# Performance work log

Measured on AMD Instinct MI355X. Metric: run time of the kernel, lower is better.

The kernel has to match this reference:

```python
import jax, jax.numpy as jnp
import numpy as np

D_MODEL = 1024
NUM_HEADS = 16
HEAD_DIM = D_MODEL // NUM_HEADS


def setup_inputs() -> dict:
    key = jax.random.key(0)
    k_x, k_wqkv, k_bqkv, k_wo, k_bo = jax.random.split(key, 5)
    s = 1.0 / np.sqrt(D_MODEL)
    return {
        "x": jax.random.normal(k_x, (4, 2048, D_MODEL), dtype=jnp.float32),
        "W_qkv": jax.random.uniform(k_wqkv, (D_MODEL, 3 * D_MODEL), jnp.float32, -s, s),
        "b_qkv": jax.random.uniform(k_bqkv, (3 * D_MODEL,), jnp.float32, -s, s),
        "W_out": jax.random.uniform(k_wo, (D_MODEL, D_MODEL), jnp.float32, -s, s),
        "b_out": jax.random.uniform(k_bo, (D_MODEL,), jnp.float32, -s, s),
    }


def reference(x, W_qkv, b_qkv, W_out, b_out):
    B, N, C = x.shape
    # fused QKV projection -> [B, N, 3, H, Dh]
    qkv = (x @ W_qkv + b_qkv).reshape(B, N, 3, NUM_HEADS, HEAD_DIM)
    q = jnp.transpose(qkv[:, :, 0], (0, 2, 1, 3))  # [B, H, N, Dh]
    k = jnp.transpose(qkv[:, :, 1], (0, 2, 1, 3))
    v = jnp.transpose(qkv[:, :, 2], (0, 2, 1, 3))
    scale = 1.0 / jnp.sqrt(jnp.asarray(HEAD_DIM, dtype=x.dtype))
    attn = jnp.einsum('bhqd,bhkd->bhqk', q, k) * scale  # [B, H, N, N]
    attn = jax.nn.softmax(attn, axis=-1)
    # dropout is identity in eval mode
    out = jnp.einsum('bhqk,bhkd->bhqd', attn, v)  # [B, H, N, Dh]
    out = jnp.transpose(out, (0, 2, 1, 3)).reshape(B, N, C)
    return out @ W_out + b_out
```

## Files before the change

kernel.cpp:

```cpp
#include <hip/hip_runtime.h>


typedef __bf16 bf16x8 __attribute__((ext_vector_type(8)));
typedef float f32x4 __attribute__((ext_vector_type(4)));
typedef unsigned int u32x4 __attribute__((ext_vector_type(4)));

#define DEV __device__ __forceinline__

DEV unsigned short f2b(float x) {
  unsigned int u = __float_as_uint(x);
  u += 0x7fffu + ((u >> 16) & 1u);
  return (unsigned short)(u >> 16);
}

DEV unsigned int pk2(float a, float b) {
  union { __bf16 h[2]; unsigned int u; } c;
  c.h[0] = (__bf16)a;
  c.h[1] = (__bf16)b;
  return c.u;
}

#if __has_builtin(__builtin_amdgcn_exp2f)
DEV float exp2_fast(float x) { return __builtin_amdgcn_exp2f(x); }
#else
DEV float exp2_fast(float x) { return exp2f(x); }
#endif

DEV void xpose_pair(unsigned int a, unsigned int b,
                    unsigned int& x, unsigned int& y) {
#if __has_builtin(__builtin_amdgcn_permlane32_swap) && \
    __has_builtin(__builtin_amdgcn_permlane16_swap)
  auto t = __builtin_amdgcn_permlane32_swap(a, b, false, false);
  auto u = __builtin_amdgcn_permlane16_swap(t[0], t[1], false, false);
  x = u[0];
  y = u[1];
#else
  int la = (int)(threadIdx.x & 63);
  unsigned int a32 = (unsigned int)__shfl_xor((int)a, 32, 64);
  unsigned int b32 = (unsigned int)__shfl_xor((int)b, 32, 64);
  unsigned int t0 = (la < 32) ? a : b32;
  unsigned int t1 = (la < 32) ? a32 : b;
  unsigned int t0x = (unsigned int)__shfl_xor((int)t0, 16, 64);
  unsigned int t1x = (unsigned int)__shfl_xor((int)t1, 16, 64);
  bool odd = ((la >> 4) & 1) != 0;
  x = odd ? t1x : t0;
  y = odd ? t1 : t0x;
#endif
}

DEV bf16x8 u4_to_bf(u32x4 v) {
  union { u32x4 u; bf16x8 b; } c;
  c.u = v;
  return c.b;
}

DEV void g2l16(const void* g, void* l) {
  __builtin_amdgcn_global_load_lds(
      (const __attribute__((address_space(1))) unsigned int*)(unsigned long long)g,
      (__attribute__((address_space(3))) unsigned int*)(unsigned int)(unsigned long long)l,
      16, 0, 0);
}

__global__ void cvt_x_kernel(const float* __restrict__ x,
                             unsigned short* __restrict__ xb) {
  int i = blockIdx.x * blockDim.x + threadIdx.x;
  float4 v = ((const float4*)x)[i];
  ushort4 o;
  o.x = f2b(v.x); o.y = f2b(v.y); o.z = f2b(v.z); o.w = f2b(v.w);
  ((ushort4*)xb)[i] = o;
}

__global__ void cvt_wt_kernel(const float* __restrict__ W,
                              unsigned short* __restrict__ Wt,
                              int K, int N) {
  __shared__ float tile[32][33];
  int n0 = blockIdx.x * 32, k0 = blockIdx.y * 32;
  int tx = threadIdx.x, ty = threadIdx.y;
#pragma unroll
  for (int i = 0; i < 32; i += 8)
    tile[ty + i][tx] = W[(size_t)(k0 + ty + i) * N + n0 + tx];
  __syncthreads();
#pragma unroll
  for (int i = 0; i < 32; i += 8)
    Wt[(size_t)(n0 + ty + i) * K + k0 + tx] = f2b(tile[tx][ty + i]);
}

#define QSCALE 0.18033688011112042f

template <int MODE>
__global__ __launch_bounds__(256, 2)
void gemm_bt_kernel(const unsigned short* __restrict__ A,
                    const unsigned short* __restrict__ Bt,
                    const float* __restrict__ bias,
                    unsigned short* __restrict__ qout,
                    unsigned short* __restrict__ kfrout,
                    unsigned short* __restrict__ vfrout,
                    float* __restrict__ fout) {
  constexpr int K = 1024;
  __shared__ unsigned short As[128 * 32];
  __shared__ unsigned short Bs[128 * 32];

  const int tid = threadIdx.x;
  const int lane = tid & 63;
  const int w = tid >> 6;
  const int wm = w & 1, wn = w >> 1;
  const int l15 = lane & 15, quad = lane >> 4;
  const int m0 = blockIdx.y * 128;
  const int n0 = blockIdx.x * 128;

  const unsigned short* Ag = A + (size_t)m0 * K;
  const unsigned short* Bg = Bt + (size_t)n0 * K;

  const int c0 = tid, c1 = tid + 256;
  const size_t ga0 = (size_t)(c0 >> 2) * K + (size_t)(c0 & 3) * 8;
  const size_t ga1 = (size_t)(c1 >> 2) * K + (size_t)(c1 & 3) * 8;
  unsigned short* la0 = &As[c0 * 8];
  unsigned short* la1 = &As[c1 * 8];
  unsigned short* lb0 = &Bs[c0 * 8];
  unsigned short* lb1 = &Bs[c1 * 8];

  f32x4 acc[4][4] = {};

  for (int kt = 0; kt < K; kt += 32) {
    g2l16(Ag + ga0 + kt, la0);
    g2l16(Ag + ga1 + kt, la1);
    g2l16(Bg + ga0 + kt, lb0);
    g2l16(Bg + ga1 + kt, lb1);
    __syncthreads();
    bf16x8 af[4], bfr[4];
#pragma unroll
    for (int i = 0; i < 4; ++i) {
      af[i]  = *(const bf16x8*)&As[(wm * 64 + i * 16 + l15) * 32 + quad * 8];
      bfr[i] = *(const bf16x8*)&Bs[(wn * 64 + i * 16 + l15) * 32 + quad * 8];
    }
#pragma unroll
    for (int mi = 0; mi < 4; ++mi)
#pragma unroll
      for (int ni = 0; ni < 4; ++ni)
        acc[mi][ni] = __builtin_amdgcn_mfma_f32_16x16x32_bf16(
            af[mi], bfr[ni], acc[mi][ni], 0, 0, 0);
    __syncthreads();
  }

  float bv[4];
#pragma unroll
  for (int ni = 0; ni < 4; ++ni)
    bv[ni] = bias[n0 + wn * 64 + ni * 16 + l15];

  if (MODE == 0) {
    const int sel = n0 >> 10;
    const int bbat = m0 >> 11;
    const int ktb = ((m0 & 2047) >> 6) + wm;
    if (sel == 0) {
#pragma unroll
      for (int mi = 0; mi < 4; ++mi) {
        int rb = m0 + wm * 64 + mi * 16 + quad * 4;
#pragma unroll
        for (int ni = 0; ni < 4; ++ni) {
          int c = (n0 & 1023) + wn * 64 + ni * 16 + l15;
#pragma unroll
          for (int r = 0; r < 4; ++r)
            qout[(size_t)(rb + r) * 1024 + c] =
                f2b((acc[mi][ni][r] + bv[ni]) * QSCALE);
        }
      }
    } else if (sel == 1) {
#pragma unroll
      for (int ni = 0; ni < 4; ++ni) {
        int c = (n0 & 1023) + wn * 64 + ni * 16 + l15;
        int h = c >> 6, d = c & 63;
        int kc = d >> 5, dq = (d >> 3) & 3, j = d & 7;
        size_t fb = ((((size_t)(bbat * 16 + h) * 32 + ktb) * 8) + kc) * 512 +
                    (size_t)(dq * 16) * 8 + j;
#pragma unroll
        for (int mi = 0; mi < 4; ++mi) {
          size_t fm = fb + (size_t)mi * 1024;
#pragma unroll
          for (int r = 0; r < 4; ++r)
            kfrout[fm + (quad * 4 + r) * 8] = f2b(acc[mi][ni][r] + bv[ni]);
        }
      }
    } else {
      const int fqb = quad >> 1;
      const int jj0 = (quad & 1) * 4;
#pragma unroll
      for (int ni = 0; ni < 4; ++ni) {
        int c = (n0 & 1023) + wn * 64 + ni * 16 + l15;
        int h = c >> 6, d = c & 63;
        int df = d >> 4, fl15 = d & 15;
#pragma unroll
        for (int mi = 0; mi < 4; ++mi) {
          int kc2 = mi >> 1;
          int fquad = (mi & 1) * 2 + fqb;
          size_t fb = ((((size_t)(bbat * 16 + h) * 32 + ktb) * 8) + df * 2 + kc2) * 512 +
                      (size_t)(fquad * 16 + fl15) * 8 + jj0;
          ushort4 pk;
          pk.x = f2b(acc[mi][ni][0] + bv[ni]);
          pk.y = f2b(acc[mi][ni][1] + bv[ni]);
          pk.z = f2b(acc[mi][ni][2] + bv[ni]);
          pk.w = f2b(acc[mi][ni][3] + bv[ni]);
          *(ushort4*)&vfrout[fb] = pk;
        }
      }
    }
  } else {
#pragma unroll
    for (int mi = 0; mi < 4; ++mi) {
      int rb = m0 + wm * 64 + mi * 16 + quad * 4;
#pragma unroll
      for (int ni = 0; ni < 4; ++ni) {
        int c = n0 + wn * 64 + ni * 16 + l15;
#pragma unroll
        for (int r = 0; r < 4; ++r)
          fout[(size_t)(rb + r) * 1024 + c] = acc[mi][ni][r] + bv[ni];
      }
    }
  }
}

__global__ __launch_bounds__(512, 1)
void attn_kernel(const unsigned short* __restrict__ qg,
                 const unsigned short* __restrict__ kfr,
                 const unsigned short* __restrict__ vfr,
                 unsigned short* __restrict__ oat) {
  __shared__ unsigned short Ks[2][4096];
  __shared__ unsigned short Vs[2][4096];

  const int tid = threadIdx.x;
  const int lane = tid & 63;
  const int w = tid >> 6;
  const int l15 = lane & 15, quad = lane >> 4;

  const int head = blockIdx.x * 8 + (blockIdx.y >> 2);
  const int q0 = (blockIdx.y & 3) * 512 + w * 64;
  const int b = head >> 4, h = head & 15;
  const size_t tokbase = (size_t)b * 2048;

  bf16x8 qf[4][2];
#pragma unroll
  for (int ni = 0; ni < 4; ++ni)
#pragma unroll
    for (int kc = 0; kc < 2; ++kc) {
      int q = q0 + ni * 16 + l15;
      qf[ni][kc] = *(const bf16x8*)(qg + (tokbase + q) * 1024 + h * 64 +
                                    kc * 32 + quad * 8);
    }

  f32x4 oacc[4][4] = {};
  float lsum[4] = {0.f, 0.f, 0.f, 0.f};

  const unsigned short* kpb = kfr + (size_t)head * 32 * 4096;
  const unsigned short* vpb = vfr + (size_t)head * 32 * 4096;

  auto stage = [&](int buf, int t) {
    g2l16(kpb + (size_t)t * 4096 + tid * 8, &Ks[buf][tid * 8]);
    g2l16(vpb + (size_t)t * 4096 + tid * 8, &Vs[buf][tid * 8]);
  };

  stage(0, 0);
  __syncthreads();

  bf16x8 kf[8], vf[8];
#pragma unroll
  for (int f = 0; f < 8; ++f)
    kf[f] = *(const bf16x8*)&Ks[0][f * 512 + lane * 8];
  stage(1, 1);

  f32x4 st[4][4];
#pragma unroll
  for (int ni = 0; ni < 4; ++ni)
#pragma unroll
    for (int mi = 0; mi < 4; ++mi)
      st[ni][mi] = (f32x4){0.f, 0.f, 0.f, 0.f};
#pragma unroll
  for (int kc = 0; kc < 2; ++kc)
#pragma unroll
    for (int mi = 0; mi < 4; ++mi)
#pragma unroll
      for (int ni = 0; ni < 4; ++ni)
        st[ni][mi] = __builtin_amdgcn_mfma_f32_16x16x32_bf16(
            kf[mi * 2 + kc], qf[ni][kc], st[ni][mi], 0, 0, 0);
#pragma unroll
  for (int f = 0; f < 8; ++f)
    vf[f] = *(const bf16x8*)&Vs[0][f * 512 + lane * 8];

  for (int t = 0; t < 32; ++t) {
    if (t < 31) {
      __syncthreads();
      const int nb = (t + 1) & 1;
#pragma unroll
      for (int f = 0; f < 8; ++f)
        kf[f] = *(const bf16x8*)&Ks[nb][f * 512 + lane * 8];
      if (t < 30) stage(t & 1, t + 2);
    }

    bf16x8 pf2[4][2];
#pragma unroll
    for (int ni = 0; ni < 4; ++ni) {
      float rs = 0.f;
      unsigned int s0[4], s1[4];
#pragma unroll
      for (int mi = 0; mi < 4; ++mi) {
        float p0 = exp2_fast(st[ni][mi][0]);
        float p1 = exp2_fast(st[ni][mi][1]);
        float p2 = exp2_fast(st[ni][mi][2]);
        float p3 = exp2_fast(st[ni][mi][3]);
        rs += (p0 + p1) + (p2 + p3);
        s0[mi] = pk2(p0, p1);
        s1[mi] = pk2(p2, p3);
      }
      lsum[ni] += rs;
      unsigned int o00, o01, o02, o03, o10, o11, o12, o13;
      xpose_pair(s0[0], s0[1], o00, o02);
      xpose_pair(s1[0], s1[1], o01, o03);
      xpose_pair(s0[2], s0[3], o10, o12);
      xpose_pair(s1[2], s1[3], o11, o13);
      u32x4 t0 = {o00, o01, o02, o03};
      u32x4 t1 = {o10, o11, o12, o13};
      pf2[ni][0] = u4_to_bf(t0);
      pf2[ni][1] = u4_to_bf(t1);
    }

    __builtin_amdgcn_s_setprio(1);
#pragma unroll
    for (int kc = 0; kc < 2; ++kc)
#pragma unroll
      for (int df = 0; df < 4; ++df)
#pragma unroll
        for (int ni = 0; ni < 4; ++ni)
          oacc[df][ni] = __builtin_amdgcn_mfma_f32_16x16x32_bf16(
              vf[df * 2 + kc], pf2[ni][kc], oacc[df][ni], 0, 0, 0);
    __builtin_amdgcn_s_setprio(0);

    if (t < 31) {
      const int nb = (t + 1) & 1;
#pragma unroll
      for (int f = 0; f < 8; ++f)
        vf[f] = *(const bf16x8*)&Vs[nb][f * 512 + lane * 8];
#pragma unroll
      for (int ni = 0; ni < 4; ++ni)
#pragma unroll
        for (int mi = 0; mi < 4; ++mi)
          st[ni][mi] = (f32x4){0.f, 0.f, 0.f, 0.f};
      __builtin_amdgcn_s_setprio(1);
#pragma unroll
      for (int kc = 0; kc < 2; ++kc)
#pragma unroll
        for (int mi = 0; mi < 4; ++mi)
#pragma unroll
          for (int ni = 0; ni < 4; ++ni)
            st[ni][mi] = __builtin_amdgcn_mfma_f32_16x16x32_bf16(
                kf[mi * 2 + kc], qf[ni][kc], st[ni][mi], 0, 0, 0);
      __builtin_amdgcn_s_setprio(0);
    }
  }

#pragma unroll
  for (int ni = 0; ni < 4; ++ni) {
    float s = lsum[ni];
    s += __shfl_xor(s, 16, 64);
    s += __shfl_xor(s, 32, 64);
    float inv = __builtin_amdgcn_rcpf(s);
    int q = q0 + ni * 16 + l15;
#pragma unroll
    for (int df = 0; df < 4; ++df) {
      uint2 pw;
      pw.x = pk2(oacc[df][ni][0] * inv, oacc[df][ni][1] * inv);
      pw.y = pk2(oacc[df][ni][2] * inv, oacc[df][ni][3] * inv);
      *(uint2*)&oat[(tokbase + q) * 1024 + h * 64 + df * 16 + quad * 4] = pw;
    }
  }
}

extern "C" void kernel_launch(void* const* d_in, const int* in_sizes, int n_in,
                              void* d_out, int out_size, void* d_ws, size_t ws_size,
                              hipStream_t stream) {
  const float* x    = (const float*)d_in[0];
  const float* Wqkv = (const float*)d_in[1];
  const float* bqkv = (const float*)d_in[2];
  const float* Wout = (const float*)d_in[3];
  const float* bout = (const float*)d_in[4];
  float* out = (float*)d_out;

  char* ws = (char*)d_ws;
  unsigned short* xb  = (unsigned short*)(ws + (size_t)0);
  unsigned short* wqt = (unsigned short*)(ws + ((size_t)16 << 20));
  unsigned short* wot = (unsigned short*)(ws + ((size_t)22 << 20));
  unsigned short* qbf = (unsigned short*)(ws + ((size_t)24 << 20));
  unsigned short* kfr = (unsigned short*)(ws + ((size_t)40 << 20));
  unsigned short* vfr = (unsigned short*)(ws + ((size_t)56 << 20));
  unsigned short* oat = (unsigned short*)(ws + ((size_t)72 << 20));

  cvt_x_kernel<<<8192, 256, 0, stream>>>(x, xb);
  cvt_wt_kernel<<<dim3(96, 32), dim3(32, 8), 0, stream>>>(Wqkv, wqt, 1024, 3072);
  cvt_wt_kernel<<<dim3(32, 32), dim3(32, 8), 0, stream>>>(Wout, wot, 1024, 1024);

  gemm_bt_kernel<0><<<dim3(24, 64), 256, 0, stream>>>(
      xb, wqt, bqkv, qbf, kfr, vfr, nullptr);

  attn_kernel<<<dim3(8, 32), 512, 0, stream>>>(qbf, kfr, vfr, oat);

  gemm_bt_kernel<1><<<dim3(8, 64), 256, 0, stream>>>(
      oat, wot, bout, nullptr, nullptr, nullptr, out);
}
```

Before: 285.9 us.

## Shrink attention blocks to 256 threads and restructure QK/softmax pipelining

The attention kernel now runs blocks of 4 waves with two blocks per CU instead of one 8-wave block, covering 256 queries per block on a doubled grid. The loop changes from computing the whole next tile's scores ahead to a per-query-group ping-pong: QK for the next 16-row group is issued while exp2 runs on the current one. V fragments are loaded per k-chunk to cut register pressure. This aims to raise occupancy and overlap MFMA with softmax math, at the cost of loading each K/V tile twice as often across the grid and losing cross-tile prefetch of scores.

New measurement: 279.7 us. 1.02x faster.

```diff
diff --git a/kernel.cpp b/kernel.cpp
--- a/kernel.cpp
+++ b/kernel.cpp
@@ -218,7 +218,7 @@
   }
 }
 
-__global__ __launch_bounds__(512, 1)
+__global__ __launch_bounds__(256, 2)
 void attn_kernel(const unsigned short* __restrict__ qg,
                  const unsigned short* __restrict__ kfr,
                  const unsigned short* __restrict__ vfr,
@@ -231,8 +231,8 @@
   const int w = tid >> 6;
   const int l15 = lane & 15, quad = lane >> 4;
 
-  const int head = blockIdx.x * 8 + (blockIdx.y >> 2);
-  const int q0 = (blockIdx.y & 3) * 512 + w * 64;
+  const int head = blockIdx.x * 8 + (blockIdx.y >> 3);
+  const int q0 = (blockIdx.y & 7) * 256 + w * 64;
   const int b = head >> 4, h = head & 15;
   const size_t tokbase = (size_t)b * 2048;
 
@@ -253,58 +253,65 @@
   const unsigned short* vpb = vfr + (size_t)head * 32 * 4096;
 
   auto stage = [&](int buf, int t) {
-    g2l16(kpb + (size_t)t * 4096 + tid * 8, &Ks[buf][tid * 8]);
-    g2l16(vpb + (size_t)t * 4096 + tid * 8, &Vs[buf][tid * 8]);
+    const unsigned short* ks = kpb + (size_t)t * 4096;
+    const unsigned short* vs = vpb + (size_t)t * 4096;
+    g2l16(ks + (size_t)tid * 8,         &Ks[buf][tid * 8]);
+    g2l16(ks + (size_t)(tid + 256) * 8, &Ks[buf][(tid + 256) * 8]);
+    g2l16(vs + (size_t)tid * 8,         &Vs[buf][tid * 8]);
+    g2l16(vs + (size_t)(tid + 256) * 8, &Vs[buf][(tid + 256) * 8]);
   };
 
   stage(0, 0);
   __syncthreads();
 
-  bf16x8 kf[8], vf[8];
-#pragma unroll
-  for (int f = 0; f < 8; ++f)
-    kf[f] = *(const bf16x8*)&Ks[0][f * 512 + lane * 8];
-  stage(1, 1);
-
-  f32x4 st[4][4];
-#pragma unroll
-  for (int ni = 0; ni < 4; ++ni)
+  const f32x4 z4 = {0.f, 0.f, 0.f, 0.f};
+
+  for (int t = 0; t < 32; ++t) {
+    const int cur = t & 1;
+    if (t < 31) stage(cur ^ 1, t + 1);
+
+    const unsigned short* Kb = Ks[cur];
+    bf16x8 kf[8];
+#pragma unroll
+    for (int f = 0; f < 8; ++f)
+      kf[f] = *(const bf16x8*)&Kb[f * 512 + lane * 8];
+
+    f32x4 st[2][4];
+    bf16x8 pf2[4][2];
+    __builtin_amdgcn_s_setprio(1);
 #pragma unroll
     for (int mi = 0; mi < 4; ++mi)
-      st[ni][mi] = (f32x4){0.f, 0.f, 0.f, 0.f};
-#pragma unroll
-  for (int kc = 0; kc < 2; ++kc)
+      st[0][mi] = __builtin_amdgcn_mfma_f32_16x16x32_bf16(
+          kf[mi * 2], qf[0][0], z4, 0, 0, 0);
 #pragma unroll
     for (int mi = 0; mi < 4; ++mi)
-#pragma unroll
-      for (int ni = 0; ni < 4; ++ni)
-        st[ni][mi] = __builtin_amdgcn_mfma_f32_16x16x32_bf16(
-            kf[mi * 2 + kc], qf[ni][kc], st[ni][mi], 0, 0, 0);
-#pragma unroll
-  for (int f = 0; f < 8; ++f)
-    vf[f] = *(const bf16x8*)&Vs[0][f * 512 + lane * 8];
-
-  for (int t = 0; t < 32; ++t) {
-    if (t < 31) {
-      __syncthreads();
-      const int nb = (t + 1) & 1;
-#pragma unroll
-      for (int f = 0; f < 8; ++f)
-        kf[f] = *(const bf16x8*)&Ks[nb][f * 512 + lane * 8];
-      if (t < 30) stage(t & 1, t + 2);
-    }
-
-    bf16x8 pf2[4][2];
+      st[0][mi] = __builtin_amdgcn_mfma_f32_16x16x32_bf16(
+          kf[mi * 2 + 1], qf[0][1], st[0][mi], 0, 0, 0);
+    __builtin_amdgcn_s_setprio(0);
+
 #pragma unroll
     for (int ni = 0; ni < 4; ++ni) {
+      const int pcur = ni & 1, pnx = pcur ^ 1;
+      if (ni < 3) {
+        __builtin_amdgcn_s_setprio(1);
+#pragma unroll
+        for (int mi = 0; mi < 4; ++mi)
+          st[pnx][mi] = __builtin_amdgcn_mfma_f32_16x16x32_bf16(
+              kf[mi * 2], qf[ni + 1][0], z4, 0, 0, 0);
+#pragma unroll
+        for (int mi = 0; mi < 4; ++mi)
+          st[pnx][mi] = __builtin_amdgcn_mfma_f32_16x16x32_bf16(
+              kf[mi * 2 + 1], qf[ni + 1][1], st[pnx][mi], 0, 0, 0);
+        __builtin_amdgcn_s_setprio(0);
+      }
       float rs = 0.f;
       unsigned int s0[4], s1[4];
 #pragma unroll
       for (int mi = 0; mi < 4; ++mi) {
-        float p0 = exp2_fast(st[ni][mi][0]);
-        float p1 = exp2_fast(st[ni][mi][1]);
-        float p2 = exp2_fast(st[ni][mi][2]);
-        float p3 = exp2_fast(st[ni][mi][3]);
+        float p0 = exp2_fast(st[pcur][mi][0]);
+        float p1 = exp2_fast(st[pcur][mi][1]);
+        float p2 = exp2_fast(st[pcur][mi][2]);
+        float p3 = exp2_fast(st[pcur][mi][3]);
         rs += (p0 + p1) + (p2 + p3);
         s0[mi] = pk2(p0, p1);
         s1[mi] = pk2(p2, p3);
@@ -321,38 +328,24 @@
       pf2[ni][1] = u4_to_bf(t1);
     }
 
-    __builtin_amdgcn_s_setprio(1);
-#pragma unroll
-    for (int kc = 0; kc < 2; ++kc)
+    const unsigned short* Vb = Vs[cur];
+#pragma unroll
+    for (int kc = 0; kc < 2; ++kc) {
+      bf16x8 vf4[4];
+#pragma unroll
+      for (int df = 0; df < 4; ++df)
+        vf4[df] = *(const bf16x8*)&Vb[(df * 2 + kc) * 512 + lane * 8];
+      __builtin_amdgcn_s_setprio(1);
 #pragma unroll
       for (int df = 0; df < 4; ++df)
 #pragma unroll
         for (int ni = 0; ni < 4; ++ni)
           oacc[df][ni] = __builtin_amdgcn_mfma_f32_16x16x32_bf16(
-              vf[df * 2 + kc], pf2[ni][kc], oacc[df][ni], 0, 0, 0);
-    __builtin_amdgcn_s_setprio(0);
-
-    if (t < 31) {
-      const int nb = (t + 1) & 1;
-#pragma unroll
-      for (int f = 0; f < 8; ++f)
-        vf[f] = *(const bf16x8*)&Vs[nb][f * 512 + lane * 8];
-#pragma unroll
-      for (int ni = 0; ni < 4; ++ni)
-#pragma unroll
-        for (int mi = 0; mi < 4; ++mi)
-          st[ni][mi] = (f32x4){0.f, 0.f, 0.f, 0.f};
-      __builtin_amdgcn_s_setprio(1);
-#pragma unroll
-      for (int kc = 0; kc < 2; ++kc)
-#pragma unroll
-        for (int mi = 0; mi < 4; ++mi)
-#pragma unroll
-          for (int ni = 0; ni < 4; ++ni)
-            st[ni][mi] = __builtin_amdgcn_mfma_f32_16x16x32_bf16(
-                kf[mi * 2 + kc], qf[ni][kc], st[ni][mi], 0, 0, 0);
+              vf4[df], pf2[ni][kc], oacc[df][ni], 0, 0, 0);
       __builtin_amdgcn_s_setprio(0);
     }
+
+    if (t < 31) __syncthreads();
   }
 
 #pragma unroll
@@ -398,7 +391,7 @@
   gemm_bt_kernel<0><<<dim3(24, 64), 256, 0, stream>>>(
       xb, wqt, bqkv, qbf, kfr, vfr, nullptr);
 
-  attn_kernel<<<dim3(8, 32), 512, 0, stream>>>(qbf, kfr, vfr, oat);
+  attn_kernel<<<dim3(8, 64), 256, 0, stream>>>(qbf, kfr, vfr, oat);
 
   gemm_bt_kernel<1><<<dim3(8, 64), 256, 0, stream>>>(
       oat, wot, bout, nullptr, nullptr, nullptr, out);
```
